# Kernel optimization log

Hardware: AMD Instinct MI355X
Metric: run time of the kernel (lower is better)

## Reference

```python
import jax, jax.numpy as jnp
import numpy as np

B = 8192          # batch_size (pairs of embeddings)
D = 1024          # embedding dim
C = 1024          # number of classes (torch.unique(labels) -> 0..C-1, all present)
EPS = 1e-12       # F.normalize eps


def _normalize(x):
    # F.normalize(x, dim=1): x / max(||x||_2, eps)
    n = jnp.linalg.norm(x, axis=1, keepdims=True)
    return x / jnp.maximum(n, EPS)


def setup_inputs() -> dict:
    key = jax.random.key(0)
    k1, k2, k3 = jax.random.split(key, 3)
    emb_i = jax.random.normal(k1, (B, D), dtype=jnp.float32)
    emb_j = jax.random.normal(k2, (B, D), dtype=jnp.float32)
    # shuffled arange % C guarantees every class id in [0, C) appears,
    # matching torch.unique(labels) == arange(C)
    labels = jax.random.permutation(k3, jnp.arange(B, dtype=jnp.int32) % C).astype(jnp.int64)
    return {"emb_i": emb_i, "emb_j": emb_j, "labels": labels}


def reference(emb_i, emb_j, labels):
    z_i = _normalize(emb_i)  # [B, D]
    z_j = _normalize(emb_j)  # [B, D]

    # vectorized replacement of the per-label python loop:
    # class_prototypes[c] = mean of z_i rows with label c  (segment mean)
    seg_sum = jax.ops.segment_sum(z_i, labels, num_segments=C)                    # [C, D]
    seg_cnt = jax.ops.segment_sum(jnp.ones((B,), z_i.dtype), labels, num_segments=C)  # [C]
    prototypes = seg_sum / seg_cnt[:, None]                                       # [C, D]

    # similarity = 2 - cdist(z_j, prototypes, p=2)
    d2 = (jnp.sum(z_j * z_j, axis=1)[:, None]
          + jnp.sum(prototypes * prototypes, axis=1)[None, :]
          - 2.0 * z_j @ prototypes.T)                                             # [B, C]
    sim = 2.0 - jnp.sqrt(jnp.maximum(d2, 0.0))

    # match_matrix: labels_proto (arange(C)) == labels[:, None]
    match = (jnp.arange(C)[None, :] == labels[:, None]).astype(sim.dtype)         # [B, C]

    # BCEWithLogitsLoss (mean reduction), numerically stable via log_sigmoid
    loss = jnp.mean(-(match * jax.nn.log_sigmoid(sim)
                      + (1.0 - match) * jax.nn.log_sigmoid(-sim)))
    return loss
```

## Files before the change

### kernel.cpp

```cpp
#include <hip/hip_runtime.h>

#define B_N 8192
#define D_N 1024
#define C_N 1024
#define BM 128
#define BN 128
#define BK 64

typedef __attribute__((ext_vector_type(8))) __bf16 bf16x8;
typedef __attribute__((ext_vector_type(4))) __bf16 bf16x4;
typedef __attribute__((ext_vector_type(4))) float floatx4;

__device__ inline unsigned short f2bf(float f) {
  union { float f; unsigned int u; } cv; cv.f = f;
  unsigned int b = cv.u;
  unsigned int r = (b + 0x7FFFu + ((b >> 16) & 1u)) >> 16;
  return (unsigned short)r;
}
__device__ inline float d4(const float4 a) {
  return a.x * a.x + a.y * a.y + a.z * a.z + a.w * a.w;
}
__device__ inline ushort4 pk4(const float4 v, const float s) {
  ushort4 u;
  u.x = f2bf(v.x * s); u.y = f2bf(v.y * s);
  u.z = f2bf(v.z * s); u.w = f2bf(v.w * s);
  return u;
}

__global__ __launch_bounds__(256) void prep_kernel(
    const float* __restrict__ emb_i, const float* __restrict__ emb_j,
    const int* __restrict__ labels,
    float* __restrict__ rn, unsigned short* __restrict__ proto,
    float* __restrict__ p2, float* __restrict__ out) {
  __shared__ float sx[4][8];
  __shared__ int list[8];
  __shared__ int scnt;

  const int t = threadIdx.x;
  const int lane = t & 63;
  const int wid = t >> 6;
  const int blk = blockIdx.x;

  if (t == 0) scnt = 0;
  if (blk == 0 && t == 0) out[0] = 0.0f;

#pragma unroll
  for (int it = 0; it < 2; ++it) {
    const int row = blk * 8 + it * 4 + wid;
    const float4* src = (const float4*)(emb_j + (size_t)row * D_N);
    float ss = d4(src[lane]) + d4(src[lane + 64]) +
               d4(src[lane + 128]) + d4(src[lane + 192]);
    for (int o = 32; o; o >>= 1) ss += __shfl_xor(ss, o, 64);
    if (lane == 0) rn[row] = 1.0f / fmaxf(sqrtf(ss), 1e-12f);
  }

  const int c = blk;
  __syncthreads();
  const int4* lab4 = (const int4*)labels;
  for (int i = 0; i < 8; ++i) {
    const int q = i * 256 + t;
    const int4 L = lab4[q];
    const int base = q * 4;
    if (L.x == c) list[atomicAdd(&scnt, 1) & 7] = base;
    if (L.y == c) list[atomicAdd(&scnt, 1) & 7] = base + 1;
    if (L.z == c) list[atomicAdd(&scnt, 1) & 7] = base + 2;
    if (L.w == c) list[atomicAdd(&scnt, 1) & 7] = base + 3;
  }
  __syncthreads();

  const float* base = emb_i + wid * 256;
  float4 v[8];
  float ss[8];
#pragma unroll
  for (int k = 0; k < 8; ++k) {
    v[k] = ((const float4*)(base + (size_t)list[k] * D_N))[lane];
    ss[k] = d4(v[k]);
  }
#pragma unroll
  for (int k = 0; k < 8; ++k)
    for (int o = 32; o; o >>= 1) ss[k] += __shfl_xor(ss[k], o, 64);
  if (lane == 0) {
#pragma unroll
    for (int k = 0; k < 8; ++k) sx[wid][k] = ss[k];
  }
  __syncthreads();

  float4 a = make_float4(0.f, 0.f, 0.f, 0.f);
#pragma unroll
  for (int k = 0; k < 8; ++k) {
    const float tot = sx[0][k] + sx[1][k] + sx[2][k] + sx[3][k];
    const float iv = 1.0f / fmaxf(sqrtf(tot), 1e-12f);
    a.x += v[k].x * iv; a.y += v[k].y * iv;
    a.z += v[k].z * iv; a.w += v[k].w * iv;
  }
  a.x *= 0.125f; a.y *= 0.125f; a.z *= 0.125f; a.w *= 0.125f;

  float pp = d4(a);
  for (int o = 32; o; o >>= 1) pp += __shfl_xor(pp, o, 64);
  __syncthreads();
  if (lane == 0) sx[wid][0] = pp;
  __syncthreads();
  if (t == 0) p2[c] = sx[0][0] + sx[1][0] + sx[2][0] + sx[3][0];

  ((ushort4*)(proto + (size_t)c * D_N + wid * 256))[lane] = pk4(a, 1.0f);
}

__global__ __launch_bounds__(256) void gemm_loss_kernel(
    const float* __restrict__ Ej,
    const unsigned short* __restrict__ P,
    const float* __restrict__ rn,
    const float* __restrict__ p2,
    const int* __restrict__ labels,
    float* __restrict__ out) {
  __shared__ __align__(16) unsigned short As[BM * BK];
  __shared__ __align__(16) unsigned short Bs[BN * BK];
  __shared__ float srn[BM];
  __shared__ float sred[4];

  const int t = threadIdx.x;
  const int lane = t & 63;
  const int wid = t >> 6;
  const int wm = (wid >> 1) * 64;
  const int wn = (wid & 1) * 64;
  const int bm = blockIdx.x;
  const int bn = blockIdx.y;

  if (t < BM) srn[t] = rn[bm * BM + t];

  floatx4 acc[4][4];
#pragma unroll
  for (int i = 0; i < 4; ++i)
#pragma unroll
    for (int j = 0; j < 4; ++j)
      acc[i][j] = (floatx4){0.f, 0.f, 0.f, 0.f};

  const int srow = t >> 3;
  const int scol = (((t & 7) ^ (srow & 7)) << 3);
  const unsigned short* Bg = P + (size_t)(bn * BN + srow) * D_N + scol;
  unsigned short* Bl = Bs + t * 8;

  const float4* Agp = (const float4*)(Ej + (size_t)(bm * BM + (t >> 4)) * D_N) + (t & 15);
  unsigned short* Aw = As + (t >> 4) * 64 +
                       ((((t & 15) >> 1) ^ ((t >> 4) & 7)) << 3) + (t & 1) * 4;

  for (int k0 = 0; k0 < D_N; k0 += BK) {
#pragma unroll
    for (int it = 0; it < 4; ++it) {
      __builtin_amdgcn_global_load_lds(
          (const __attribute__((address_space(1))) void*)(Bg + (size_t)it * 32 * D_N + k0),
          (__attribute__((address_space(3))) void*)(Bl + it * 2048), 16, 0, 0);
    }
    const int kq = k0 >> 2;
#pragma unroll
    for (int k = 0; k < 8; ++k) {
      const float4 w = Agp[k * 4096 + kq];
      bf16x4 bv;
      bv[0] = (__bf16)w.x; bv[1] = (__bf16)w.y;
      bv[2] = (__bf16)w.z; bv[3] = (__bf16)w.w;
      *(bf16x4*)(Aw + k * 1024) = bv;
    }
    __syncthreads();
#pragma unroll
    for (int kk = 0; kk < BK; kk += 32) {
      const int swz = ((((kk >> 3) + (lane >> 4)) ^ (lane & 7)) << 3);
      bf16x8 af[4], bfr[4];
#pragma unroll
      for (int mi = 0; mi < 4; ++mi)
        af[mi] = *(const bf16x8*)(As + (wm + mi * 16 + (lane & 15)) * BK + swz);
#pragma unroll
      for (int ni = 0; ni < 4; ++ni)
        bfr[ni] = *(const bf16x8*)(Bs + (wn + ni * 16 + (lane & 15)) * BK + swz);
#pragma unroll
      for (int mi = 0; mi < 4; ++mi)
#pragma unroll
        for (int ni = 0; ni < 4; ++ni)
          acc[mi][ni] = __builtin_amdgcn_mfma_f32_16x16x32_bf16(af[mi], bfr[ni], acc[mi][ni], 0, 0, 0);
    }
    __syncthreads();
  }

  const int colb = bn * BN + wn + (lane & 15);
  const int rowloc = wm + ((lane >> 4) << 2);
  float p2c[4];
#pragma unroll
  for (int ni = 0; ni < 4; ++ni) p2c[ni] = p2[colb + ni * 16];

  float lsum = 0.f;
#pragma unroll
  for (int mi = 0; mi < 4; ++mi) {
#pragma unroll
    for (int r = 0; r < 4; ++r) {
      const int rl = rowloc + mi * 16 + r;
      const float rv = srn[rl];
      const int lab = labels[bm * BM + rl];
#pragma unroll
      for (int ni = 0; ni < 4; ++ni) {
        const float dot = acc[mi][ni][r] * rv;
        const float d2 = 1.0f + p2c[ni] - 2.0f * dot;
        const float s = 2.0f - sqrtf(fmaxf(d2, 0.0f));
        const float sp = fmaxf(s, 0.0f) + log1pf(expf(-fabsf(s)));
        lsum += sp - ((lab == colb + ni * 16) ? s : 0.0f);
      }
    }
  }
  for (int o = 32; o; o >>= 1) lsum += __shfl_xor(lsum, o, 64);
  if (lane == 0) sred[wid] = lsum;
  __syncthreads();
  if (t == 0)
    atomicAdd(out, (sred[0] + sred[1] + sred[2] + sred[3]) *
                       (1.0f / ((float)B_N * (float)C_N)));
}

extern "C" void kernel_launch(void* const* d_in, const int* in_sizes, int n_in,
                              void* d_out, int out_size, void* d_ws, size_t ws_size,
                              hipStream_t stream) {
  const float* emb_i = (const float*)d_in[0];
  const float* emb_j = (const float*)d_in[1];
  const int* labels = (const int*)d_in[2];
  float* out = (float*)d_out;

  char* ws = (char*)d_ws;
  float* rn = (float*)ws;
  unsigned short* proto = (unsigned short*)(ws + (size_t)32768);
  float* p2 = (float*)(ws + (size_t)32768 + 2097152);

  prep_kernel<<<dim3(C_N), 256, 0, stream>>>(emb_i, emb_j, labels, rn,
                                             proto, p2, out);
  gemm_loss_kernel<<<dim3(B_N / BM, C_N / BN), 256, 0, stream>>>(emb_j, proto,
                                                                 rn, p2, labels, out);
}
```

Baseline: 151.9 us.

## Fuse emb_j row-norm computation into GEMM A-tile loads and halve BM

Removes the emb_j norm pass from the prep kernel and computes each row's sum of squares inside the GEMM while loading and converting the A tile, then reduces it across lanes before the loss epilogue. BM drops from 128 to 64, which doubles the grid and halves the per-wave accumulator count. The intent is to avoid a separate 32 MB read of emb_j and to improve occupancy. In exchange, each B tile is now loaded by twice as many blocks and per-block MFMA reuse is lower.

```diff
diff --git a/kernel.cpp b/kernel.cpp
--- a/kernel.cpp
+++ b/kernel.cpp
@@ -3,7 +3,7 @@
 #define B_N 8192
 #define D_N 1024
 #define C_N 1024
-#define BM 128
+#define BM 64
 #define BN 128
 #define BK 64
 
@@ -28,10 +28,9 @@
 }
 
 __global__ __launch_bounds__(256) void prep_kernel(
-    const float* __restrict__ emb_i, const float* __restrict__ emb_j,
-    const int* __restrict__ labels,
-    float* __restrict__ rn, unsigned short* __restrict__ proto,
-    float* __restrict__ p2, float* __restrict__ out) {
+    const float* __restrict__ emb_i, const int* __restrict__ labels,
+    unsigned short* __restrict__ proto, float* __restrict__ p2,
+    float* __restrict__ out) {
   __shared__ float sx[4][8];
   __shared__ int list[8];
   __shared__ int scnt;
@@ -39,23 +38,12 @@
   const int t = threadIdx.x;
   const int lane = t & 63;
   const int wid = t >> 6;
-  const int blk = blockIdx.x;
+  const int c = blockIdx.x;
 
   if (t == 0) scnt = 0;
-  if (blk == 0 && t == 0) out[0] = 0.0f;
-
-#pragma unroll
-  for (int it = 0; it < 2; ++it) {
-    const int row = blk * 8 + it * 4 + wid;
-    const float4* src = (const float4*)(emb_j + (size_t)row * D_N);
-    float ss = d4(src[lane]) + d4(src[lane + 64]) +
-               d4(src[lane + 128]) + d4(src[lane + 192]);
-    for (int o = 32; o; o >>= 1) ss += __shfl_xor(ss, o, 64);
-    if (lane == 0) rn[row] = 1.0f / fmaxf(sqrtf(ss), 1e-12f);
-  }
-
-  const int c = blk;
-  __syncthreads();
+  if (c == 0 && t == 0) out[0] = 0.0f;
+  __syncthreads();
+
   const int4* lab4 = (const int4*)labels;
   for (int i = 0; i < 8; ++i) {
     const int q = i * 256 + t;
@@ -108,7 +96,6 @@
 __global__ __launch_bounds__(256) void gemm_loss_kernel(
     const float* __restrict__ Ej,
     const unsigned short* __restrict__ P,
-    const float* __restrict__ rn,
     const float* __restrict__ p2,
     const int* __restrict__ labels,
     float* __restrict__ out) {
@@ -120,16 +107,14 @@
   const int t = threadIdx.x;
   const int lane = t & 63;
   const int wid = t >> 6;
-  const int wm = (wid >> 1) * 64;
+  const int wm = (wid >> 1) * 32;
   const int wn = (wid & 1) * 64;
   const int bm = blockIdx.x;
   const int bn = blockIdx.y;
 
-  if (t < BM) srn[t] = rn[bm * BM + t];
-
-  floatx4 acc[4][4];
-#pragma unroll
-  for (int i = 0; i < 4; ++i)
+  floatx4 acc[2][4];
+#pragma unroll
+  for (int i = 0; i < 2; ++i)
 #pragma unroll
     for (int j = 0; j < 4; ++j)
       acc[i][j] = (floatx4){0.f, 0.f, 0.f, 0.f};
@@ -143,6 +128,8 @@
   unsigned short* Aw = As + (t >> 4) * 64 +
                        ((((t & 15) >> 1) ^ ((t >> 4) & 7)) << 3) + (t & 1) * 4;
 
+  float ssr[4] = {0.f, 0.f, 0.f, 0.f};
+
   for (int k0 = 0; k0 < D_N; k0 += BK) {
 #pragma unroll
     for (int it = 0; it < 4; ++it) {
@@ -152,8 +139,9 @@
     }
     const int kq = k0 >> 2;
 #pragma unroll
-    for (int k = 0; k < 8; ++k) {
+    for (int k = 0; k < 4; ++k) {
       const float4 w = Agp[k * 4096 + kq];
+      ssr[k] += d4(w);
       bf16x4 bv;
       bv[0] = (__bf16)w.x; bv[1] = (__bf16)w.y;
       bv[2] = (__bf16)w.z; bv[3] = (__bf16)w.w;
@@ -163,21 +151,35 @@
 #pragma unroll
     for (int kk = 0; kk < BK; kk += 32) {
       const int swz = ((((kk >> 3) + (lane >> 4)) ^ (lane & 7)) << 3);
-      bf16x8 af[4], bfr[4];
-#pragma unroll
-      for (int mi = 0; mi < 4; ++mi)
+      bf16x8 af[2], bfr[4];
+#pragma unroll
+      for (int mi = 0; mi < 2; ++mi)
         af[mi] = *(const bf16x8*)(As + (wm + mi * 16 + (lane & 15)) * BK + swz);
 #pragma unroll
       for (int ni = 0; ni < 4; ++ni)
         bfr[ni] = *(const bf16x8*)(Bs + (wn + ni * 16 + (lane & 15)) * BK + swz);
 #pragma unroll
-      for (int mi = 0; mi < 4; ++mi)
+      for (int mi = 0; mi < 2; ++mi)
 #pragma unroll
         for (int ni = 0; ni < 4; ++ni)
           acc[mi][ni] = __builtin_amdgcn_mfma_f32_16x16x32_bf16(af[mi], bfr[ni], acc[mi][ni], 0, 0, 0);
     }
     __syncthreads();
   }
+
+#pragma unroll
+  for (int k = 0; k < 4; ++k) {
+    ssr[k] += __shfl_xor(ssr[k], 1, 64);
+    ssr[k] += __shfl_xor(ssr[k], 2, 64);
+    ssr[k] += __shfl_xor(ssr[k], 4, 64);
+    ssr[k] += __shfl_xor(ssr[k], 8, 64);
+  }
+  if ((t & 15) == 0) {
+#pragma unroll
+    for (int k = 0; k < 4; ++k)
+      srn[(t >> 4) + 16 * k] = 1.0f / fmaxf(sqrtf(ssr[k]), 1e-12f);
+  }
+  __syncthreads();
 
   const int colb = bn * BN + wn + (lane & 15);
   const int rowloc = wm + ((lane >> 4) << 2);
@@ -187,7 +189,7 @@
 
   float lsum = 0.f;
 #pragma unroll
-  for (int mi = 0; mi < 4; ++mi) {
+  for (int mi = 0; mi < 2; ++mi) {
 #pragma unroll
     for (int r = 0; r < 4; ++r) {
       const int rl = rowloc + mi * 16 + r;
@@ -220,12 +222,10 @@
   float* out = (float*)d_out;
 
   char* ws = (char*)d_ws;
-  float* rn = (float*)ws;
-  unsigned short* proto = (unsigned short*)(ws + (size_t)32768);
-  float* p2 = (float*)(ws + (size_t)32768 + 2097152);
-
-  prep_kernel<<<dim3(C_N), 256, 0, stream>>>(emb_i, emb_j, labels, rn,
-                                             proto, p2, out);
+  unsigned short* proto = (unsigned short*)ws;
+  float* p2 = (float*)(ws + (size_t)2097152);
+
+  prep_kernel<<<dim3(C_N), 256, 0, stream>>>(emb_i, labels, proto, p2, out);
   gemm_loss_kernel<<<dim3(B_N / BM, C_N / BN), 256, 0, stream>>>(emb_j, proto,
-                                                                 rn, p2, labels, out);
-}
+                                                                 p2, labels, out);
+}
```

Result: no change. 154.3 us (+1.5%).
